# Optimization experiments

Measured on AMD Instinct MI355X. Metric: run time of the kernel, lower is better.

Reference implementation:

```python
import jax, jax.numpy as jnp
import numpy as np

D_MODEL = 768
D_STATE = 64
HEADDIM = 8
EXPAND = 2
D_CONV = 4
CHUNK = 128
D_INNER = EXPAND * D_MODEL            # 1536
NHEADS = D_INNER // HEADDIM           # 192
CONV_DIM = D_INNER + 2 * D_STATE      # 1664 (ngroups=1)
D_IN_PROJ = 2 * D_INNER + 2 * D_STATE + NHEADS  # 3392
BATCH = 2
SEQLEN = 1024


def setup_inputs() -> dict:
    key = jax.random.key(0)
    ks = jax.random.split(key, 8)
    x = jax.random.normal(ks[0], (BATCH, D_MODEL, SEQLEN), jnp.float32)
    W_in = jax.random.normal(ks[1], (D_IN_PROJ, D_MODEL), jnp.float32) / np.sqrt(D_MODEL)
    conv_w = jax.random.normal(ks[2], (CONV_DIM, D_CONV), jnp.float32) / np.sqrt(D_CONV)
    conv_b = jnp.zeros((CONV_DIM,), jnp.float32)
    # dt bias init: inverse softplus of dt ~ LogUniform[1e-3, 0.1] (mamba2 default)
    dt = jnp.exp(jax.random.uniform(ks[3], (NHEADS,)) * (np.log(0.1) - np.log(1e-3)) + np.log(1e-3))
    dt_bias = dt + jnp.log(-jnp.expm1(-dt))
    # A ~ Uniform[1.0, 1.1] per A_init_range, stored as log
    A_log = jnp.log(jax.random.uniform(ks[4], (NHEADS,), minval=1.0, maxval=1.1))
    D = jnp.ones((NHEADS,), jnp.float32)
    norm_w = jnp.ones((D_INNER,), jnp.float32)
    W_out = jax.random.normal(ks[5], (D_MODEL, D_INNER), jnp.float32) / np.sqrt(D_INNER)
    return dict(x=x, W_in=W_in, conv_w=conv_w, conv_b=conv_b, dt_bias=dt_bias,
                A_log=A_log, D=D, norm_w=norm_w, W_out=W_out)


def _segsum(t):
    # t: (..., T) -> (..., T, T) with [i,j] = sum_{k=j+1..i} t_k (i>=j), -inf above diag
    T = t.shape[-1]
    cs = jnp.cumsum(t, axis=-1)
    d = cs[..., :, None] - cs[..., None, :]
    mask = jnp.tril(jnp.ones((T, T), bool))
    return jnp.where(mask, d, -jnp.inf)


def _ssd(xh, dt, A, Bm, Cm):
    # xh: (b,l,h,p), dt: (b,l,h), A: (h,), Bm/Cm: (b,l,n) (ngroups=1)
    b, l, h, p = xh.shape
    c = l // CHUNK
    xh = xh.reshape(b, c, CHUNK, h, p)
    dt = dt.reshape(b, c, CHUNK, h)
    Bm = Bm.reshape(b, c, CHUNK, -1)
    Cm = Cm.reshape(b, c, CHUNK, -1)
    dA = jnp.transpose(dt * A, (0, 3, 1, 2))          # (b,h,c,Q)
    A_cs = jnp.cumsum(dA, axis=-1)                    # (b,h,c,Q)
    Lmat = jnp.exp(_segsum(dA))                       # (b,h,c,Q,Q) causal decay
    xdt = xh * dt[..., None]                          # (b,c,Q,h,p)
    # intra-chunk (diagonal blocks)
    scores = jnp.einsum('bcln,bcsn->bcls', Cm, Bm)
    Y_diag = jnp.einsum('bcls,bhcls,bcshp->bclhp', scores, Lmat, xdt)
    # chunk-final states
    decay_states = jnp.exp(A_cs[..., -1:] - A_cs)     # (b,h,c,Q)
    states = jnp.einsum('bcln,bhcl,bclhp->bchpn', Bm, decay_states, xdt)
    states = jnp.concatenate([jnp.zeros_like(states[:, :1]), states], axis=1)  # (b,c+1,h,p,n)
    # inter-chunk recurrence via decay matrix over chunks (c is small)
    dA_chunk = jnp.pad(A_cs[..., -1], ((0, 0), (0, 0), (1, 0)))  # (b,h,c+1)
    decay_chunk = jnp.exp(_segsum(dA_chunk))                     # (b,h,c+1,c+1)
    new_states = jnp.einsum('bhzc,bchpn->bzhpn', decay_chunk, states)
    prev = new_states[:, :-1]                         # (b,c,h,p,n) state entering each chunk
    Y_off = jnp.einsum('bcln,bchpn,bhcl->bclhp', Cm, prev, jnp.exp(A_cs))
    return (Y_diag + Y_off).reshape(b, l, h, p)


def _forward(x, W_in, conv_w, conv_b, dt_bias, A_log, D, norm_w, W_out):
    u = jnp.transpose(x, (0, 2, 1))                   # (b,l,d_model)
    zxbcdt = u @ W_in.T                               # (b,l,3392)
    z = zxbcdt[..., :D_INNER]
    xBC = zxbcdt[..., D_INNER:D_INNER + CONV_DIM]
    dt = jax.nn.softplus(zxbcdt[..., -NHEADS:] + dt_bias)
    # causal depthwise conv1d + silu
    xc = jnp.transpose(xBC, (0, 2, 1))                # (b,conv_dim,l)
    xc = jax.lax.conv_general_dilated(xc, conv_w[:, None, :], (1,),
                                      [(D_CONV - 1, 0)], feature_group_count=CONV_DIM)
    xBC = jax.nn.silu(jnp.transpose(xc, (0, 2, 1)) + conv_b)
    xs = xBC[..., :D_INNER]
    Bm = xBC[..., D_INNER:D_INNER + D_STATE]
    Cm = xBC[..., -D_STATE:]
    A = -jnp.exp(A_log)
    b, l, _ = xs.shape
    xh = xs.reshape(b, l, NHEADS, HEADDIM)
    y = _ssd(xh, dt, A, Bm, Cm) + D[None, None, :, None] * xh
    y = y.reshape(b, l, D_INNER)
    # RMSNormGated (norm_before_gate=False): gate then rmsnorm
    y = y * jax.nn.silu(z)
    y = y * jax.lax.rsqrt(jnp.mean(y * y, axis=-1, keepdims=True) + 1e-5) * norm_w
    out = y @ W_out.T
    return jnp.transpose(out, (0, 2, 1))              # back to (b, d_model, l)


def reference(x, W_in, conv_w, conv_b, dt_bias, A_log, D, norm_w, W_out):
    return _forward(x, W_in, conv_w, conv_b, dt_bias, A_log, D, norm_w, W_out)
```

## Files before the change

### kernel.cpp

```cpp
#include <hip/hip_runtime.h>
#include <cstddef>
#include <cstdint>


typedef __bf16 bf16_t;
typedef bf16_t bf16x2 __attribute__((ext_vector_type(2)));
typedef bf16_t bf16x4 __attribute__((ext_vector_type(4)));
typedef bf16_t bf16x8 __attribute__((ext_vector_type(8)));
typedef float f32x4 __attribute__((ext_vector_type(4)));

#define OFF_UB   ((size_t)0)
#define OFF_ZX   (OFF_UB  + 786432)
#define OFF_XBC  (OFF_ZX  + 3276800)
#define OFF_DT   (OFF_XBC + 1703936)
#define OFF_ACS  (OFF_DT  + 393216)
#define OFF_SC   (OFF_ACS + 393216)
#define OFF_ST   (OFF_SC  + 262144)
#define OFF_PV   (OFF_ST  + 1572864)
#define OFF_Y    (OFF_PV  + 786432)
#define OFF_Y2B  (OFF_Y   + 1572864)

__device__ __forceinline__ float siluf(float x) { return x / (1.f + __expf(-x)); }

__global__ __launch_bounds__(256) void transpose_x_kernel(const float* __restrict__ x,
                                                          bf16_t* __restrict__ ub) {
  __shared__ float tile[32][33];
  int b = blockIdx.z;
  int d0 = blockIdx.x * 32, l0 = blockIdx.y * 32;
  int tx = threadIdx.x & 31, ty = threadIdx.x >> 5;
  for (int r = ty; r < 32; r += 8)
    tile[r][tx] = x[((size_t)(b * 768 + d0 + r)) * 1024 + l0 + tx];
  __syncthreads();
  for (int r = ty; r < 32; r += 8)
    ub[((size_t)(b * 1024 + l0 + r)) * 768 + d0 + tx] = (bf16_t)tile[tx][r];
}

template <int TMF, int MODE>
__global__ __launch_bounds__(256) void gemm_fused(const bf16_t* __restrict__ A,
                                                  const float* __restrict__ B32,
                                                  void* __restrict__ Cv,
                                                  float* __restrict__ dtb,
                                                  const float* __restrict__ dt_bias,
                                                  int K) {
  constexpr int RB = TMF * 32;
  constexpr int NA = RB / 32;
  constexpr int STG = (RB * 64 + 128 * 64) / 2;
  constexpr int SMEMN = (STG > 4256) ? STG : 4256;
  __shared__ __align__(16) float smemf[SMEMN];
  bf16_t* Asmem = (bf16_t*)smemf;
  bf16_t* Bsmem = Asmem + RB * 64;
  float* eps = smemf;

  int tid = threadIdx.x;
  int wave = tid >> 6, lane = tid & 63;
  int wr = wave >> 1, wc = wave & 1;

  int gx = gridDim.x, gy = gridDim.y;
  int nwg = gx * gy;
  int flat = blockIdx.y * gx + blockIdx.x;
  int q = nwg >> 3;
  int cm = (flat & 7) * q + (flat >> 3);
  int bx = cm / gy, by = cm % gy;
  int m0 = by * RB, n0 = bx * 128;

  const bf16_t* Ag = A + (size_t)m0 * K;

  int aofs[NA]; const bf16_t* agp[NA];
#pragma unroll
  for (int i = 0; i < NA; ++i) {
    int id = i * 256 + tid;
    int r = id >> 3, c = id & 7;
    aofs[i] = r * 128 + ((c ^ (r & 7)) << 4);
    agp[i] = Ag + (size_t)r * K + c * 8;
  }
  int bofs[4]; const float* bgp[4]; bool bval[4];
#pragma unroll
  for (int i = 0; i < 4; ++i) {
    int id = i * 256 + tid;
    int r = id >> 3, c = id & 7;
    bofs[i] = r * 128 + ((c ^ (r & 7)) << 4);
    int grow = n0 + r;
    bval[i] = (MODE == 1) || (grow < 3392);
    bgp[i] = B32 + (size_t)grow * K + c * 8;
  }

  f32x4 acc[TMF][4] = {};
  uint4 areg[NA];
  float4 b0[4], b1[4];
#pragma unroll
  for (int i = 0; i < NA; ++i) areg[i] = *(const uint4*)(agp[i]);
#pragma unroll
  for (int i = 0; i < 4; ++i) {
    if (bval[i]) {
      b0[i] = *(const float4*)(bgp[i]);
      b1[i] = *(const float4*)(bgp[i] + 4);
    } else {
      b0[i] = make_float4(0.f, 0.f, 0.f, 0.f);
      b1[i] = make_float4(0.f, 0.f, 0.f, 0.f);
    }
  }

  for (int k0 = 0; k0 < K; k0 += 64) {
    __syncthreads();
#pragma unroll
    for (int i = 0; i < NA; ++i) *(uint4*)((char*)Asmem + aofs[i]) = areg[i];
#pragma unroll
    for (int i = 0; i < 4; ++i) {
      bf16x8 o = {(bf16_t)b0[i].x, (bf16_t)b0[i].y, (bf16_t)b0[i].z, (bf16_t)b0[i].w,
                  (bf16_t)b1[i].x, (bf16_t)b1[i].y, (bf16_t)b1[i].z, (bf16_t)b1[i].w};
      *(bf16x8*)((char*)Bsmem + bofs[i]) = o;
    }
    __syncthreads();
    if (k0 + 64 < K) {
#pragma unroll
      for (int i = 0; i < NA; ++i) areg[i] = *(const uint4*)(agp[i] + k0 + 64);
#pragma unroll
      for (int i = 0; i < 4; ++i) {
        if (bval[i]) {
          b0[i] = *(const float4*)(bgp[i] + k0 + 64);
          b1[i] = *(const float4*)(bgp[i] + k0 + 68);
        }
      }
    }
#pragma unroll
    for (int half = 0; half < 2; ++half) {
      int kk = half * 32;
      int ca = (kk >> 3) + (lane >> 4);
      bf16x8 af[TMF], bfr[4];
#pragma unroll
      for (int f = 0; f < TMF; ++f) {
        int Ra = wr * (TMF * 16) + f * 16 + (lane & 15);
        af[f] = *(const bf16x8*)((const char*)Asmem + Ra * 128 + ((ca ^ (Ra & 7)) << 4));
      }
#pragma unroll
      for (int f = 0; f < 4; ++f) {
        int Rb = wc * 64 + f * 16 + (lane & 15);
        bfr[f] = *(const bf16x8*)((const char*)Bsmem + Rb * 128 + ((ca ^ (Rb & 7)) << 4));
      }
#pragma unroll
      for (int i = 0; i < TMF; ++i)
#pragma unroll
        for (int j = 0; j < 4; ++j)
          acc[i][j] = __builtin_amdgcn_mfma_f32_16x16x32_bf16(af[i], bfr[j], acc[i][j], 0, 0, 0);
    }
  }

#pragma unroll
  for (int p = 0; p < RB / 32; ++p) {
    __syncthreads();
#pragma unroll
    for (int i = 0; i < TMF; ++i) {
      int rg = wr * (TMF * 16) + i * 16;
      if ((rg >> 5) == p) {
        int rl = (rg & 31) + ((lane >> 4) << 2);
#pragma unroll
        for (int j = 0; j < 4; ++j) {
          int col = wc * 64 + j * 16 + (lane & 15);
#pragma unroll
          for (int rr = 0; rr < 4; ++rr)
            eps[(rl + rr) * 133 + col] = acc[i][j][rr];
        }
      }
    }
    __syncthreads();
    if (MODE == 0) {
      if (n0 < 3200) {
        bf16_t* Cb = (bf16_t*)Cv;
#pragma unroll
        for (int r = 0; r < 4; ++r) {
          int idx = tid + r * 256;
          int row = idx >> 5, c4 = (idx & 31) << 2;
          float4 v = *(const float4*)&eps[row * 133 + c4];
          bf16x4 o = {(bf16_t)v.x, (bf16_t)v.y, (bf16_t)v.z, (bf16_t)v.w};
          *(bf16x4*)&Cb[(size_t)(m0 + p * 32 + row) * 3200 + n0 + c4] = o;
        }
      } else {
        int b = m0 >> 10, t0 = (m0 & 1023) + p * 32;
#pragma unroll
        for (int cg = 0; cg < 4; ++cg) {
          int col = cg * 32 + (tid >> 3);
          int h = n0 + col - 3200;
          if (h < 192) {
            int rr = (tid & 7) * 4;
            float bias = dt_bias[h];
            float vv[4];
#pragma unroll
            for (int k = 0; k < 4; ++k) {
              float v = eps[(rr + k) * 133 + col] + bias;
              vv[k] = (v > 20.f) ? v : log1pf(__expf(v));
            }
            *(float4*)&dtb[((size_t)(b * 192 + h)) * 1024 + t0 + rr] =
                make_float4(vv[0], vv[1], vv[2], vv[3]);
          }
        }
      }
    } else {
      float* Cf = (float*)Cv;
      int b = m0 >> 10, l0 = (m0 & 1023) + p * 32;
#pragma unroll
      for (int cg = 0; cg < 4; ++cg) {
        int col = cg * 32 + (tid >> 3);
        int rr = (tid & 7) * 4;
        float4 v = make_float4(eps[(rr + 0) * 133 + col], eps[(rr + 1) * 133 + col],
                               eps[(rr + 2) * 133 + col], eps[(rr + 3) * 133 + col]);
        *(float4*)&Cf[((size_t)(b * 768 + n0 + col)) * 1024 + l0 + rr] = v;
      }
    }
  }
}

__global__ __launch_bounds__(128) void conv_kernel(const bf16_t* __restrict__ zxb,
                                                   const float* __restrict__ conv_w,
                                                   const float* __restrict__ conv_b,
                                                   bf16_t* __restrict__ xBC) {
  int ch2 = blockIdx.x * 128 + threadIdx.x;
  if (ch2 >= 832) return;
  int ch = ch2 * 2;
  int m = blockIdx.y;
  int b = m >> 10, l = m & 1023;
  float a0 = conv_b[ch], a1 = conv_b[ch + 1];
  const bf16_t* base = zxb + (size_t)b * 1024 * 3200 + 1536 + ch;
#pragma unroll
  for (int j = 0; j < 4; ++j) {
    int tj = l - 3 + j;
    if (tj >= 0) {
      bf16x2 v = *(const bf16x2*)&base[(size_t)tj * 3200];
      a0 = fmaf(conv_w[ch * 4 + j], (float)v[0], a0);
      a1 = fmaf(conv_w[(ch + 1) * 4 + j], (float)v[1], a1);
    }
  }
  bf16x2 o = {(bf16_t)siluf(a0), (bf16_t)siluf(a1)};
  *(bf16x2*)&xBC[(size_t)m * 1664 + ch] = o;
}

__global__ __launch_bounds__(128) void scan_kernel(const float* __restrict__ dtb,
                                                   const float* __restrict__ A_log,
                                                   float* __restrict__ Acs) {
  __shared__ float s[128];
  int idx = blockIdx.x;
  int c = idx & 7;
  int bh = idx >> 3;
  int h = bh % 192;
  int l = threadIdx.x;
  float Ah = -__expf(A_log[h]);
  float v = dtb[(size_t)bh * 1024 + c * 128 + l] * Ah;
  s[l] = v;
  __syncthreads();
  for (int off = 1; off < 128; off <<= 1) {
    float add = (l >= off) ? s[l - off] : 0.f;
    __syncthreads();
    s[l] += add;
    __syncthreads();
  }
  Acs[(size_t)idx * 128 + l] = s[l];
}

__global__ __launch_bounds__(256) void scores_kernel(const bf16_t* __restrict__ xBC,
                                                     float* __restrict__ scores) {
  __shared__ float Cs[16][16];
  __shared__ float Bs[16][128];
  int bc = blockIdx.x;
  int l0 = blockIdx.y * 16;
  const bf16_t* base = xBC + (size_t)bc * 128 * 1664;
  int tid = threadIdx.x;
  int tx = tid & 15, ty = tid >> 4;
  float acc[8] = {};
  for (int n0 = 0; n0 < 64; n0 += 16) {
    Cs[tid & 15][tid >> 4] =
        (float)base[(size_t)(l0 + (tid >> 4)) * 1664 + 1600 + n0 + (tid & 15)];
    for (int id = tid; id < 2048; id += 256) {
      int sr = id >> 4, nn = id & 15;
      Bs[nn][sr] = (float)base[(size_t)sr * 1664 + 1536 + n0 + nn];
    }
    __syncthreads();
#pragma unroll
    for (int nn = 0; nn < 16; ++nn) {
      float a = Cs[nn][ty];
#pragma unroll
      for (int j = 0; j < 8; ++j)
        acc[j] = fmaf(a, Bs[nn][tx * 8 + j], acc[j]);
    }
    __syncthreads();
  }
  float* srow = scores + (size_t)bc * 16384 + (size_t)(l0 + ty) * 128;
#pragma unroll
  for (int j = 0; j < 8; ++j) srow[tx * 8 + j] = acc[j];
}

__global__ __launch_bounds__(256) void states_mfma_kernel(
    const bf16_t* __restrict__ xBC, const float* __restrict__ dtb,
    const float* __restrict__ Acs, float* __restrict__ st2) {
  __shared__ bf16_t Asm[64 * 128];
  __shared__ bf16_t Wsm[128 * 128];
  __shared__ float dcoef[16][128];
  int tile = blockIdx.x;
  int bc = blockIdx.y;
  int c = bc & 7, b = bc >> 3;
  int hg0 = tile * 16;
  int tid = threadIdx.x;
  int wave = tid >> 6, lane = tid & 63;

#pragma unroll
  for (int i = 0; i < 8; ++i) {
    int id = tid + i * 256;
    int hh = id >> 7, s = id & 127;
    int h = hg0 + hh;
    const float* ar = Acs + (((size_t)(b * 192 + h)) * 8 + c) * 128;
    float dv = dtb[((size_t)(b * 192 + h)) * 1024 + c * 128 + s];
    dcoef[hh][s] = dv * __expf(ar[127] - ar[s]);
  }
#pragma unroll
  for (int i = 0; i < 32; ++i) {
    int id = tid + i * 256;
    int s = id >> 6, n = id & 63;
    float v = (float)xBC[((size_t)(bc * 128 + s)) * 1664 + 1536 + n];
    int byte = n * 256 + (((s >> 3) ^ (n & 7)) << 4) + (s & 7) * 2;
    *(bf16_t*)((char*)Asm + byte) = (bf16_t)v;
  }
  __syncthreads();
#pragma unroll
  for (int i = 0; i < 64; ++i) {
    int id = tid + i * 256;
    int s = id >> 7, hp = id & 127;
    float v = (float)xBC[((size_t)(bc * 128 + s)) * 1664 + hg0 * 8 + hp] * dcoef[hp >> 3][s];
    int byte = hp * 256 + (((s >> 3) ^ (hp & 7)) << 4) + (s & 7) * 2;
    *(bf16_t*)((char*)Wsm + byte) = (bf16_t)v;
  }
  __syncthreads();

  f32x4 acc[4][2] = {};
#pragma unroll
  for (int ks = 0; ks < 4; ++ks) {
    int cc = ks * 4 + (lane >> 4);
    bf16x8 af[4], bfr[2];
#pragma unroll
    for (int i = 0; i < 4; ++i) {
      int Ra = i * 16 + (lane & 15);
      af[i] = *(const bf16x8*)((const char*)Asm + Ra * 256 + ((cc ^ (Ra & 7)) << 4));
    }
#pragma unroll
    for (int j = 0; j < 2; ++j) {
      int Rb = wave * 32 + j * 16 + (lane & 15);
      bfr[j] = *(const bf16x8*)((const char*)Wsm + Rb * 256 + ((cc ^ (Rb & 7)) << 4));
    }
#pragma unroll
    for (int i = 0; i < 4; ++i)
#pragma unroll
      for (int j = 0; j < 2; ++j)
        acc[i][j] = __builtin_amdgcn_mfma_f32_16x16x32_bf16(af[i], bfr[j], acc[i][j], 0, 0, 0);
  }
#pragma unroll
  for (int i = 0; i < 4; ++i)
#pragma unroll
    for (int j = 0; j < 2; ++j) {
      int n = i * 16 + ((lane >> 4) << 2);
      int col = tile * 128 + wave * 32 + j * 16 + (lane & 15);
      float* sp = st2 + (size_t)bc * 98304 + (size_t)n * 1536 + col;
#pragma unroll
      for (int rr = 0; rr < 4; ++rr) sp[(size_t)rr * 1536] = acc[i][j][rr];
    }
}

__global__ __launch_bounds__(512) void recur_kernel(const float* __restrict__ Acs,
                                                    const float* __restrict__ states,
                                                    bf16_t* __restrict__ prev) {
  int bh = blockIdx.x;
  int b = bh / 192, h = bh % 192;
  int tid = threadIdx.x;
  int p = tid >> 6, n = tid & 63;
  float s_run = 0.f;
  for (int c = 0; c < 8; ++c) {
    size_t base = (size_t)(b * 8 + c) * 98304;
    prev[base + (size_t)(h * 8 + p) * 64 + n] = (bf16_t)s_run;
    float dAs = Acs[(((size_t)(b * 192 + h)) * 8 + c) * 128 + 127];
    s_run = s_run * __expf(dAs) + states[base + (size_t)n * 1536 + h * 8 + p];
  }
}

__global__ __launch_bounds__(128) void ydiag_off_kernel(
    const bf16_t* __restrict__ xBC, const float* __restrict__ dtb,
    const float* __restrict__ Acs, const float* __restrict__ scores,
    const bf16_t* __restrict__ pv, const float* __restrict__ Dvec,
    bf16_t* __restrict__ Y) {
  __shared__ float sc_s[128][36];
  __shared__ float xdtT[8][132];
  __shared__ float acs_s[128];
  __shared__ bf16_t pv_s[512];
  int idx = blockIdx.x;
  int h = idx % 192;
  int bc = idx / 192;
  int c = bc & 7, b = bc >> 3;
  int tid = threadIdx.x;
  int lane = tid & 63, wid = tid >> 6;

  acs_s[tid] = Acs[(((size_t)(b * 192 + h)) * 8 + c) * 128 + tid];
  {
    int p = tid & 7, s0 = (tid >> 3) * 8;
    const float* dtr = dtb + ((size_t)(b * 192 + h)) * 1024 + c * 128;
#pragma unroll
    for (int j = 0; j < 8; ++j) {
      int s = s0 + j;
      xdtT[p][s] = (float)xBC[((size_t)(bc * 128 + s)) * 1664 + h * 8 + p] * dtr[s];
    }
  }
  {
    const bf16_t* pb = pv + (size_t)bc * 98304 + (size_t)h * 512;
    *(bf16x4*)&pv_s[tid * 4] = *(const bf16x4*)&pb[tid * 4];
  }

  f32x4 acc[4] = {};
  const float* sall = scores + (size_t)bc * 16384;
  for (int ks = 0; ks < 4; ++ks) {
    __syncthreads();
#pragma unroll
    for (int i = 0; i < 8; ++i) {
      int id = tid + i * 128;
      int l = id >> 3, c4 = (id & 7) * 4;
      *(float4*)&sc_s[l][c4] = *(const float4*)&sall[(size_t)l * 128 + ks * 32 + c4];
    }
    __syncthreads();

    bf16x8 bfv;
    {
      int p = lane & 7;
      int sb = (lane >> 4) * 8;
      float4 v0 = *(const float4*)&xdtT[p][ks * 32 + sb];
      float4 v1 = *(const float4*)&xdtT[p][ks * 32 + sb + 4];
      bfv[0] = (bf16_t)v0.x; bfv[1] = (bf16_t)v0.y; bfv[2] = (bf16_t)v0.z; bfv[3] = (bf16_t)v0.w;
      bfv[4] = (bf16_t)v1.x; bfv[5] = (bf16_t)v1.y; bfv[6] = (bf16_t)v1.z; bfv[7] = (bf16_t)v1.w;
    }
#pragma unroll
    for (int mf = 0; mf < 4; ++mf) {
      int lbase = (mf * 2 + wid) * 16;
      if (ks * 32 > lbase + 15) continue;
      int l = lbase + (lane & 15);
      float al = acs_s[l];
      int sb = (lane >> 4) * 8;
      int sg = ks * 32 + sb;
      float4 s0 = *(const float4*)&sc_s[l][sb];
      float4 s1 = *(const float4*)&sc_s[l][sb + 4];
      float4 e0 = *(const float4*)&acs_s[sg];
      float4 e1 = *(const float4*)&acs_s[sg + 4];
      float sv[8] = {s0.x, s0.y, s0.z, s0.w, s1.x, s1.y, s1.z, s1.w};
      float ev[8] = {e0.x, e0.y, e0.z, e0.w, e1.x, e1.y, e1.z, e1.w};
      bf16x8 af;
#pragma unroll
      for (int j = 0; j < 8; ++j) {
        float v = sv[j] * __expf(al - ev[j]);
        af[j] = (bf16_t)((sg + j <= l) ? v : 0.f);
      }
      acc[mf] = __builtin_amdgcn_mfma_f32_16x16x32_bf16(af, bfv, acc[mf], 0, 0, 0);
    }
  }

  __syncthreads();
#pragma unroll
  for (int ks2 = 0; ks2 < 2; ++ks2) {
    int kbase = ks2 * 32 + (lane >> 4) * 8;
    bf16x8 bv;
    {
      int p = lane & 15;
      if (p < 8) {
        bv = *(const bf16x8*)&pv_s[p * 64 + kbase];
      } else {
        bv = (bf16x8)(bf16_t)0.f;
      }
    }
#pragma unroll
    for (int mf = 0; mf < 4; ++mf) {
      int l = (mf * 2 + wid) * 16 + (lane & 15);
      float el = __expf(acs_s[l]);
      bf16x8 c8 = *(const bf16x8*)&xBC[((size_t)(bc * 128 + l)) * 1664 + 1600 + kbase];
      bf16x8 af;
#pragma unroll
      for (int j = 0; j < 8; ++j) af[j] = (bf16_t)((float)c8[j] * el);
      acc[mf] = __builtin_amdgcn_mfma_f32_16x16x32_bf16(af, bv, acc[mf], 0, 0, 0);
    }
  }

  int p = lane & 15;
  if (p < 8) {
    float Dh = Dvec[h];
    int rg = (lane >> 4) * 4;
#pragma unroll
    for (int mf = 0; mf < 4; ++mf) {
      int lbase = (mf * 2 + wid) * 16;
      bf16_t* yp = Y + ((size_t)(bc * 128 + lbase + rg)) * 1536 + h * 8 + p;
#pragma unroll
      for (int rr = 0; rr < 4; ++rr) {
        float xv = (float)xBC[((size_t)(bc * 128 + lbase + rg + rr)) * 1664 + h * 8 + p];
        yp[(size_t)rr * 1536] = (bf16_t)(acc[mf][rr] + Dh * xv);
      }
    }
  }
}

__global__ __launch_bounds__(256) void gatenorm_kernel(const bf16_t* __restrict__ Yb,
                                                       const bf16_t* __restrict__ zxb,
                                                       const float* __restrict__ norm_w,
                                                       bf16_t* __restrict__ y2b) {
  int m = blockIdx.x;
  int tid = threadIdx.x;
  int base = tid * 6;
  const bf16_t* yrow = Yb + (size_t)m * 1536 + base;
  const bf16_t* zrow = zxb + (size_t)m * 3200 + base;
  float vals[6];
  float ss = 0.f;
#pragma unroll
  for (int j = 0; j < 3; ++j) {
    bf16x2 yv = *(const bf16x2*)&yrow[j * 2];
    bf16x2 zv = *(const bf16x2*)&zrow[j * 2];
    float v0 = (float)yv[0] * siluf((float)zv[0]);
    float v1 = (float)yv[1] * siluf((float)zv[1]);
    vals[j * 2] = v0; vals[j * 2 + 1] = v1;
    ss = fmaf(v0, v0, fmaf(v1, v1, ss));
  }
#pragma unroll
  for (int off = 32; off > 0; off >>= 1) ss += __shfl_down(ss, off);
  __shared__ float red[4];
  int lane = tid & 63, wid = tid >> 6;
  if (lane == 0) red[wid] = ss;
  __syncthreads();
  float tot = red[0] + red[1] + red[2] + red[3];
  float scale = rsqrtf(tot * (1.f / 1536.f) + 1e-5f);
  bf16_t* orow = y2b + (size_t)m * 1536 + base;
#pragma unroll
  for (int j = 0; j < 3; ++j) {
    bf16x2 o = {(bf16_t)(vals[j * 2] * scale * norm_w[base + j * 2]),
                (bf16_t)(vals[j * 2 + 1] * scale * norm_w[base + j * 2 + 1])};
    *(bf16x2*)&orow[j * 2] = o;
  }
}

extern "C" void kernel_launch(void* const* d_in, const int* in_sizes, int n_in,
                              void* d_out, int out_size, void* d_ws, size_t ws_size,
                              hipStream_t stream) {
  const float* x = (const float*)d_in[0];
  const float* W_in = (const float*)d_in[1];
  const float* conv_w = (const float*)d_in[2];
  const float* conv_b = (const float*)d_in[3];
  const float* dt_bias = (const float*)d_in[4];
  const float* A_log = (const float*)d_in[5];
  const float* Dvec = (const float*)d_in[6];
  const float* norm_w = (const float*)d_in[7];
  const float* W_out = (const float*)d_in[8];
  float* out = (float*)d_out;
  float* ws = (float*)d_ws;

  bf16_t* ub = (bf16_t*)(ws + OFF_UB);
  bf16_t* zxb = (bf16_t*)(ws + OFF_ZX);
  bf16_t* xBC = (bf16_t*)(ws + OFF_XBC);
  float* dtb = ws + OFF_DT;
  float* Acs = ws + OFF_ACS;
  float* sc = ws + OFF_SC;
  float* st = ws + OFF_ST;
  bf16_t* pv = (bf16_t*)(ws + OFF_PV);
  bf16_t* Yb = (bf16_t*)(ws + OFF_Y);
  bf16_t* y2b = (bf16_t*)(ws + OFF_Y2B);

  transpose_x_kernel<<<dim3(24, 32, 2), 256, 0, stream>>>(x, ub);
  gemm_fused<1, 0><<<dim3(27, 64), 256, 0, stream>>>(ub, W_in, zxb, dtb, dt_bias, 768);
  conv_kernel<<<dim3(7, 2048), 128, 0, stream>>>(zxb, conv_w, conv_b, xBC);
  scan_kernel<<<3072, 128, 0, stream>>>(dtb, A_log, Acs);
  scores_kernel<<<dim3(16, 8), 256, 0, stream>>>(xBC, sc);
  states_mfma_kernel<<<dim3(12, 16), 256, 0, stream>>>(xBC, dtb, Acs, st);
  recur_kernel<<<384, 512, 0, stream>>>(Acs, st, pv);
  ydiag_off_kernel<<<3072, 128, 0, stream>>>(xBC, dtb, Acs, sc, pv, Dvec, Yb);
  gatenorm_kernel<<<2048, 256, 0, stream>>>(Yb, zxb, norm_w, y2b);
  gemm_fused<1, 1><<<dim3(6, 64), 256, 0, stream>>>(y2b, W_out, out, nullptr, nullptr, 1536);
}
```

Before: 161.8 us.

## Split-K the output projection GEMM and merge partials with a transpose kernel

The output projection GEMM is split along K into two halves via blockIdx.z, doubling the workgroup count from 384 to 768 to fill more CUs. Each half writes row-major fp32 partials to a new workspace buffer with coalesced float4 stores. A separate merge kernel sums the two partials and transposes them into the (b, d_model, l) output. The cost is an extra kernel launch plus a round trip of two fp32 partial buffers through memory.

```diff
diff --git a/kernel.cpp b/kernel.cpp
--- a/kernel.cpp
+++ b/kernel.cpp
@@ -19,6 +19,7 @@
 #define OFF_PV   (OFF_ST  + 1572864)
 #define OFF_Y    (OFF_PV  + 786432)
 #define OFF_Y2B  (OFF_Y   + 1572864)
+#define OFF_PB   (OFF_Y2B + 1572864)
 
 __device__ __forceinline__ float siluf(float x) { return x / (1.f + __expf(-x)); }
 
@@ -41,7 +42,7 @@
                                                   void* __restrict__ Cv,
                                                   float* __restrict__ dtb,
                                                   const float* __restrict__ dt_bias,
-                                                  int K) {
+                                                  int K, int ldk) {
   constexpr int RB = TMF * 32;
   constexpr int NA = RB / 32;
   constexpr int STG = (RB * 64 + 128 * 64) / 2;
@@ -62,8 +63,10 @@
   int cm = (flat & 7) * q + (flat >> 3);
   int bx = cm / gy, by = cm % gy;
   int m0 = by * RB, n0 = bx * 128;
-
-  const bf16_t* Ag = A + (size_t)m0 * K;
+  int kz = blockIdx.z;
+
+  const bf16_t* Ag = A + (size_t)kz * K + (size_t)m0 * ldk;
+  const float* Bz = B32 + (size_t)kz * K;
 
   int aofs[NA]; const bf16_t* agp[NA];
 #pragma unroll
@@ -71,7 +74,7 @@
     int id = i * 256 + tid;
     int r = id >> 3, c = id & 7;
     aofs[i] = r * 128 + ((c ^ (r & 7)) << 4);
-    agp[i] = Ag + (size_t)r * K + c * 8;
+    agp[i] = Ag + (size_t)r * ldk + c * 8;
   }
   int bofs[4]; const float* bgp[4]; bool bval[4];
 #pragma unroll
@@ -81,7 +84,7 @@
     bofs[i] = r * 128 + ((c ^ (r & 7)) << 4);
     int grow = n0 + r;
     bval[i] = (MODE == 1) || (grow < 3392);
-    bgp[i] = B32 + (size_t)grow * K + c * 8;
+    bgp[i] = Bz + (size_t)grow * ldk + c * 8;
   }
 
   f32x4 acc[TMF][4] = {};
@@ -195,18 +198,33 @@
         }
       }
     } else {
-      float* Cf = (float*)Cv;
-      int b = m0 >> 10, l0 = (m0 & 1023) + p * 32;
-#pragma unroll
-      for (int cg = 0; cg < 4; ++cg) {
-        int col = cg * 32 + (tid >> 3);
-        int rr = (tid & 7) * 4;
-        float4 v = make_float4(eps[(rr + 0) * 133 + col], eps[(rr + 1) * 133 + col],
-                               eps[(rr + 2) * 133 + col], eps[(rr + 3) * 133 + col]);
-        *(float4*)&Cf[((size_t)(b * 768 + n0 + col)) * 1024 + l0 + rr] = v;
-      }
-    }
-  }
+      float* Cf = (float*)Cv + (size_t)kz * 1572864;
+#pragma unroll
+      for (int r = 0; r < 4; ++r) {
+        int idx = tid + r * 256;
+        int row = idx >> 5, c4 = (idx & 31) << 2;
+        float4 v = *(const float4*)&eps[row * 133 + c4];
+        *(float4*)&Cf[(size_t)(m0 + p * 32 + row) * 768 + n0 + c4] = v;
+      }
+    }
+  }
+}
+
+__global__ __launch_bounds__(256) void merge_out_kernel(const float* __restrict__ pb,
+                                                        float* __restrict__ out) {
+  __shared__ float tile[32][33];
+  int b = blockIdx.z;
+  int d0 = blockIdx.x * 32, l0 = blockIdx.y * 32;
+  int tx = threadIdx.x & 31, ty = threadIdx.x >> 5;
+  const float* p0 = pb;
+  const float* p1 = pb + 1572864;
+  for (int r = ty; r < 32; r += 8) {
+    size_t o = (size_t)(b * 1024 + l0 + r) * 768 + d0 + tx;
+    tile[r][tx] = p0[o] + p1[o];
+  }
+  __syncthreads();
+  for (int r = ty; r < 32; r += 8)
+    out[((size_t)(b * 768 + d0 + r)) * 1024 + l0 + tx] = tile[tx][r];
 }
 
 __global__ __launch_bounds__(128) void conv_kernel(const bf16_t* __restrict__ zxb,
@@ -557,9 +575,10 @@
   bf16_t* pv = (bf16_t*)(ws + OFF_PV);
   bf16_t* Yb = (bf16_t*)(ws + OFF_Y);
   bf16_t* y2b = (bf16_t*)(ws + OFF_Y2B);
+  float* pb = ws + OFF_PB;
 
   transpose_x_kernel<<<dim3(24, 32, 2), 256, 0, stream>>>(x, ub);
-  gemm_fused<1, 0><<<dim3(27, 64), 256, 0, stream>>>(ub, W_in, zxb, dtb, dt_bias, 768);
+  gemm_fused<1, 0><<<dim3(27, 64), 256, 0, stream>>>(ub, W_in, zxb, dtb, dt_bias, 768, 768);
   conv_kernel<<<dim3(7, 2048), 128, 0, stream>>>(zxb, conv_w, conv_b, xBC);
   scan_kernel<<<3072, 128, 0, stream>>>(dtb, A_log, Acs);
   scores_kernel<<<dim3(16, 8), 256, 0, stream>>>(xBC, sc);
@@ -567,5 +586,6 @@
   recur_kernel<<<384, 512, 0, stream>>>(Acs, st, pv);
   ydiag_off_kernel<<<3072, 128, 0, stream>>>(xBC, dtb, Acs, sc, pv, Dvec, Yb);
   gatenorm_kernel<<<2048, 256, 0, stream>>>(Yb, zxb, norm_w, y2b);
-  gemm_fused<1, 1><<<dim3(6, 64), 256, 0, stream>>>(y2b, W_out, out, nullptr, nullptr, 1536);
-}
+  gemm_fused<1, 1><<<dim3(6, 64, 2), 256, 0, stream>>>(y2b, W_out, pb, nullptr, nullptr, 768, 1536);
+  merge_out_kernel<<<dim3(24, 32, 2), 256, 0, stream>>>(pb, out);
+}
```

Result: no change. 163.5 us (+1.1%).
